# Kernel optimization log

Measured on AMD Instinct MI355X. Metric: run time of the kernel, lower is better.

Reference implementation:

```python
import jax, jax.numpy as jnp
import numpy as np

HOUSE_DIM = 4
HOUSE_NUM = 10   # house_num(6) + 2*housd_num(2) for model 'HousE'
HOUSD_NUM = 2
THRED = 0.5
GAMMA = 12.0
NENTITY = 100000
NRELATION = 500
HID = 100        # hidden_dim(400) / house_dim(4)
B, NEG = 512, 256
SCALE = (GAMMA + 2.0) / (HID * HOUSE_DIM ** 0.5)  # embedding_range


def setup_inputs() -> dict:
    key = jax.random.key(0)
    ks = jax.random.split(key, 9)
    return {
        'entity_embedding': jax.random.normal(ks[0], (NENTITY, HID, HOUSE_DIM), jnp.float32) * SCALE,
        'relation_embedding': jax.random.normal(ks[1], (NRELATION, HID, HOUSE_DIM * HOUSE_NUM), jnp.float32) * SCALE,
        'k_dir_head': jax.random.uniform(ks[2], (NRELATION, 1, HOUSD_NUM), jnp.float32, -0.01, 0.01),
        'k_dir_tail': jax.random.uniform(ks[3], (NRELATION, 1, HOUSD_NUM), jnp.float32, -0.01, 0.01),
        'k_scale_head': jax.random.uniform(ks[4], (NRELATION, HID, HOUSD_NUM), jnp.float32, -1.0, 1.0),
        'k_scale_tail': jax.random.uniform(ks[5], (NRELATION, HID, HOUSD_NUM), jnp.float32, -1.0, 1.0),
        'head_idx': jax.random.randint(ks[6], (B,), 0, NENTITY, jnp.int32),
        'rel_idx': jax.random.randint(ks[7], (B,), 0, NRELATION, jnp.int32),
        'tail_idx': jax.random.randint(ks[8], (B, NEG), 0, NENTITY, jnp.int32),
    }


def _reflect(x, v, coef):
    # x - coef * <v, x> * v along the house_dim axis
    return x - coef * jnp.sum(v * x, axis=-1, keepdims=True) * v


def reference(entity_embedding, relation_embedding, k_dir_head, k_dir_tail,
              k_scale_head, k_scale_tail, head_idx, rel_idx, tail_idx):
    # norm_embedding: per-chunk L2 normalize over house_dim
    r = relation_embedding.reshape(NRELATION, HID, HOUSE_NUM, HOUSE_DIM)
    r = r / jnp.maximum(jnp.linalg.norm(r, axis=-1, keepdims=True), 1e-12)
    # k = dir * |scale|, clamp values above thred (upper clamp only)
    k_head = jnp.minimum(k_dir_head * jnp.abs(k_scale_head), THRED)  # [R, HID, housd]
    k_tail = jnp.minimum(k_dir_tail * jnp.abs(k_scale_tail), THRED)

    # tail-batch gathers
    head = entity_embedding[head_idx][:, None]   # [B, 1,   HID, hd]
    rel = r[rel_idx][:, None]                    # [B, 1,   HID, HN, hd]
    kh = k_head[rel_idx][:, None]                # [B, 1,   HID, housd]
    kt = k_tail[rel_idx][:, None]
    tail = entity_embedding[tail_idx]            # [B, NEG, HID, hd]

    # HousE scoring, tail-batch branch
    for i in range(HOUSD_NUM):
        head = _reflect(head, rel[..., HOUSE_NUM - 1 - i, :], kh[..., i:i + 1])
    for i in range(HOUSD_NUM, HOUSE_NUM - HOUSD_NUM):
        j = HOUSE_NUM - 1 - i
        head = _reflect(head, rel[..., j, :], 2.0)
    for i in range(HOUSD_NUM):
        tail = _reflect(tail, rel[..., i, :], kt[..., i:i + 1])

    diff = head - tail                            # [B, NEG, HID, hd]
    cos_score = jnp.sum(jnp.linalg.norm(diff, axis=-1), axis=-1)  # [B, NEG]
    return GAMMA - cos_score
```

## Files before the change

kernel.cpp:

```cpp
#include <hip/hip_runtime.h>
#include <math.h>

#define NENTITY   100000
#define NRELATION 500
#define HID       100
#define HOUSE_DIM 4
#define HOUSE_NUM 10
#define B_SZ      512
#define NEG       256
#define THRED     0.5f
#define GAMMA     12.0f

#define SEGS           4
#define NEG_PER_BLOCK  (NEG / SEGS)
#define BLOCK          256
#define NEG_PER_WAVE   (NEG_PER_BLOCK / 4)

__device__ __forceinline__ float dot4(const float4 a, const float4 b) {
    return a.x * b.x + a.y * b.y + a.z * b.z + a.w * b.w;
}

__device__ __forceinline__ float4 norm4(float4 v) {
    const float n = fmaxf(sqrtf(dot4(v, v)), 1e-12f);
    const float inv = 1.0f / n;
    v.x *= inv; v.y *= inv; v.z *= inv; v.w *= inv;
    return v;
}

__device__ __forceinline__ float4 reflect4(float4 x, const float4 v, const float coef) {
    const float s = coef * dot4(v, x);
    x.x -= s * v.x; x.y -= s * v.y; x.z -= s * v.z; x.w -= s * v.w;
    return x;
}

__device__ __forceinline__ float hdist(float4 tv, const float4 v0, const float4 v1,
                                       const float2 kt, const float4 hd) {
    const float s0 = kt.x * dot4(v0, tv);
    tv.x -= s0 * v0.x; tv.y -= s0 * v0.y; tv.z -= s0 * v0.z; tv.w -= s0 * v0.w;
    const float s1 = kt.y * dot4(v1, tv);
    tv.x -= s1 * v1.x; tv.y -= s1 * v1.y; tv.z -= s1 * v1.z; tv.w -= s1 * v1.w;
    const float dx = hd.x - tv.x;
    const float dy = hd.y - tv.y;
    const float dz = hd.z - tv.z;
    const float dw = hd.w - tv.w;
    return sqrtf(dx * dx + dy * dy + dz * dz + dw * dw);
}

__global__ __launch_bounds__(BLOCK, 6) void house_score_kernel(
    const float* __restrict__ ent,
    const float* __restrict__ rel,
    const float* __restrict__ kdh,
    const float* __restrict__ kdt,
    const float* __restrict__ ksh,
    const float* __restrict__ kst,
    const int* __restrict__ head_idx,
    const int* __restrict__ rel_idx,
    const int* __restrict__ tail_idx,
    float* __restrict__ out)
{
    __shared__ float4 sHead[HID];
    __shared__ float4 sV0[HID];
    __shared__ float4 sV1[HID];
    __shared__ float2 sKt[HID];

    const int blk = blockIdx.x;
    const int b   = blk >> 2;
    const int seg = blk & (SEGS - 1);
    const int tid = threadIdx.x;
    const int r   = rel_idx[b];

    if (tid < HID) {
        const int h = tid;
        const float4* rr = (const float4*)(rel + ((size_t)r * HID + h) * (HOUSE_NUM * HOUSE_DIM));

        const int he = head_idx[b];
        float4 hd = ((const float4*)ent)[(size_t)he * HID + h];

        const float kh0 = fminf(kdh[r * 2 + 0] * fabsf(ksh[((size_t)r * HID + h) * 2 + 0]), THRED);
        const float kh1 = fminf(kdh[r * 2 + 1] * fabsf(ksh[((size_t)r * HID + h) * 2 + 1]), THRED);

        hd = reflect4(hd, norm4(rr[9]), kh0);
        hd = reflect4(hd, norm4(rr[8]), kh1);
        #pragma unroll
        for (int j = 7; j >= 2; --j) hd = reflect4(hd, norm4(rr[j]), 2.0f);

        const float kt0 = fminf(kdt[r * 2 + 0] * fabsf(kst[((size_t)r * HID + h) * 2 + 0]), THRED);
        const float kt1 = fminf(kdt[r * 2 + 1] * fabsf(kst[((size_t)r * HID + h) * 2 + 1]), THRED);

        sHead[h] = hd;
        sV0[h]   = norm4(rr[0]);
        sV1[h]   = norm4(rr[1]);
        sKt[h]   = make_float2(kt0, kt1);
    }
    __syncthreads();

    const int w = tid >> 6;
    const int l = tid & 63;

    const float4 hd1 = sHead[l];
    const float4 v01 = sV0[l];
    const float4 v11 = sV1[l];
    const float2 k1  = sKt[l];
    const int   l2   = (l < 36) ? (64 + l) : 99;
    const float4 hd2 = sHead[l2];
    const float4 v02 = sV0[l2];
    const float4 v12 = sV1[l2];
    const float2 k2  = sKt[l2];
    const bool has2  = (l < 36);

    const int negbase = seg * NEG_PER_BLOCK + w * NEG_PER_WAVE;

    int my_e = 0;
    if (l < NEG_PER_WAVE) my_e = tail_idx[(size_t)b * NEG + negbase + l];

    const float4* entf4 = (const float4*)ent;

    #pragma unroll 4
    for (int i = 0; i < NEG_PER_WAVE; ++i) {
        const int e = __shfl(my_e, i);
        const float4* row = entf4 + (size_t)e * HID;

        const float4 t1 = row[l];
        float d2 = 0.0f;
        if (has2) {
            const float4 t2 = row[64 + l];
            d2 = hdist(t2, v02, v12, k2, hd2);
        }
        float s = hdist(t1, v01, v11, k1, hd1) + d2;

        #pragma unroll
        for (int m = 1; m < 64; m <<= 1) s += __shfl_xor(s, m);

        if (l == 0) out[(size_t)b * NEG + negbase + i] = GAMMA - s;
    }
}

extern "C" void kernel_launch(void* const* d_in, const int* in_sizes, int n_in,
                              void* d_out, int out_size, void* d_ws, size_t ws_size,
                              hipStream_t stream) {
    const float* ent = (const float*)d_in[0];
    const float* rel = (const float*)d_in[1];
    const float* kdh = (const float*)d_in[2];
    const float* kdt = (const float*)d_in[3];
    const float* ksh = (const float*)d_in[4];
    const float* kst = (const float*)d_in[5];
    const int* head_idx = (const int*)d_in[6];
    const int* rel_idx  = (const int*)d_in[7];
    const int* tail_idx = (const int*)d_in[8];
    float* out = (float*)d_out;

    house_score_kernel<<<B_SZ * SEGS, BLOCK, 0, stream>>>(
        ent, rel, kdh, kdt, ksh, kst, head_idx, rel_idx, tail_idx, out);
}
```

Baseline: 243.2 us.

## Split head/relation preprocessing into separate prep kernel writing workspace

Per-batch head reflection and relation normalization move into a separate prep kernel that writes results to global workspace. Before, each of the four segment blocks per batch row redid this work. The scoring kernel now reads these values directly from global memory, with no shared memory and no block barrier, and launch bounds are raised to 8 blocks per CU. The cost is an extra kernel launch, a global round trip for the precomputed data, and redundant global loads per wave in place of shared-memory reads.

```diff
diff --git a/kernel.cpp b/kernel.cpp
--- a/kernel.cpp
+++ b/kernel.cpp
@@ -15,6 +15,8 @@
 #define NEG_PER_BLOCK  (NEG / SEGS)
 #define BLOCK          256
 #define NEG_PER_WAVE   (NEG_PER_BLOCK / 4)
+
+#define WS_F4_STRIDE (B_SZ * HID)
 
 __device__ __forceinline__ float dot4(const float4 a, const float4 b) {
     return a.x * b.x + a.y * b.y + a.z * b.z + a.w * b.w;
@@ -46,7 +48,7 @@
     return sqrtf(dx * dx + dy * dy + dz * dz + dw * dw);
 }
 
-__global__ __launch_bounds__(BLOCK, 6) void house_score_kernel(
+__global__ __launch_bounds__(128) void house_prep_kernel(
     const float* __restrict__ ent,
     const float* __restrict__ rel,
     const float* __restrict__ kdh,
@@ -55,57 +57,70 @@
     const float* __restrict__ kst,
     const int* __restrict__ head_idx,
     const int* __restrict__ rel_idx,
+    float* __restrict__ ws)
+{
+    const int b = blockIdx.x;
+    const int h = threadIdx.x;
+    if (h >= HID) return;
+    const int r = rel_idx[b];
+
+    const float4* rr = (const float4*)(rel + ((size_t)r * HID + h) * (HOUSE_NUM * HOUSE_DIM));
+
+    const int he = head_idx[b];
+    float4 hd = ((const float4*)ent)[(size_t)he * HID + h];
+
+    const float kh0 = fminf(kdh[r * 2 + 0] * fabsf(ksh[((size_t)r * HID + h) * 2 + 0]), THRED);
+    const float kh1 = fminf(kdh[r * 2 + 1] * fabsf(ksh[((size_t)r * HID + h) * 2 + 1]), THRED);
+
+    hd = reflect4(hd, norm4(rr[9]), kh0);
+    hd = reflect4(hd, norm4(rr[8]), kh1);
+    #pragma unroll
+    for (int j = 7; j >= 2; --j) hd = reflect4(hd, norm4(rr[j]), 2.0f);
+
+    const float kt0 = fminf(kdt[r * 2 + 0] * fabsf(kst[((size_t)r * HID + h) * 2 + 0]), THRED);
+    const float kt1 = fminf(kdt[r * 2 + 1] * fabsf(kst[((size_t)r * HID + h) * 2 + 1]), THRED);
+
+    float4* wsHead = (float4*)ws;
+    float4* wsV0   = wsHead + WS_F4_STRIDE;
+    float4* wsV1   = wsV0 + WS_F4_STRIDE;
+    float2* wsKt   = (float2*)(wsV1 + WS_F4_STRIDE);
+
+    const int idx = b * HID + h;
+    wsHead[idx] = hd;
+    wsV0[idx]   = norm4(rr[0]);
+    wsV1[idx]   = norm4(rr[1]);
+    wsKt[idx]   = make_float2(kt0, kt1);
+}
+
+__global__ __launch_bounds__(BLOCK, 8) void house_score_kernel(
+    const float* __restrict__ ent,
     const int* __restrict__ tail_idx,
+    const float* __restrict__ ws,
     float* __restrict__ out)
 {
-    __shared__ float4 sHead[HID];
-    __shared__ float4 sV0[HID];
-    __shared__ float4 sV1[HID];
-    __shared__ float2 sKt[HID];
-
     const int blk = blockIdx.x;
     const int b   = blk >> 2;
     const int seg = blk & (SEGS - 1);
     const int tid = threadIdx.x;
-    const int r   = rel_idx[b];
-
-    if (tid < HID) {
-        const int h = tid;
-        const float4* rr = (const float4*)(rel + ((size_t)r * HID + h) * (HOUSE_NUM * HOUSE_DIM));
-
-        const int he = head_idx[b];
-        float4 hd = ((const float4*)ent)[(size_t)he * HID + h];
-
-        const float kh0 = fminf(kdh[r * 2 + 0] * fabsf(ksh[((size_t)r * HID + h) * 2 + 0]), THRED);
-        const float kh1 = fminf(kdh[r * 2 + 1] * fabsf(ksh[((size_t)r * HID + h) * 2 + 1]), THRED);
-
-        hd = reflect4(hd, norm4(rr[9]), kh0);
-        hd = reflect4(hd, norm4(rr[8]), kh1);
-        #pragma unroll
-        for (int j = 7; j >= 2; --j) hd = reflect4(hd, norm4(rr[j]), 2.0f);
-
-        const float kt0 = fminf(kdt[r * 2 + 0] * fabsf(kst[((size_t)r * HID + h) * 2 + 0]), THRED);
-        const float kt1 = fminf(kdt[r * 2 + 1] * fabsf(kst[((size_t)r * HID + h) * 2 + 1]), THRED);
-
-        sHead[h] = hd;
-        sV0[h]   = norm4(rr[0]);
-        sV1[h]   = norm4(rr[1]);
-        sKt[h]   = make_float2(kt0, kt1);
-    }
-    __syncthreads();
-
     const int w = tid >> 6;
     const int l = tid & 63;
 
-    const float4 hd1 = sHead[l];
-    const float4 v01 = sV0[l];
-    const float4 v11 = sV1[l];
-    const float2 k1  = sKt[l];
+    const float4* wsHead = (const float4*)ws;
+    const float4* wsV0   = wsHead + WS_F4_STRIDE;
+    const float4* wsV1   = wsV0 + WS_F4_STRIDE;
+    const float2* wsKt   = (const float2*)(wsV1 + WS_F4_STRIDE);
+
+    const int i1 = b * HID + l;
+    const float4 hd1 = wsHead[i1];
+    const float4 v01 = wsV0[i1];
+    const float4 v11 = wsV1[i1];
+    const float2 k1  = wsKt[i1];
     const int   l2   = (l < 36) ? (64 + l) : 99;
-    const float4 hd2 = sHead[l2];
-    const float4 v02 = sV0[l2];
-    const float4 v12 = sV1[l2];
-    const float2 k2  = sKt[l2];
+    const int   i2   = b * HID + l2;
+    const float4 hd2 = wsHead[i2];
+    const float4 v02 = wsV0[i2];
+    const float4 v12 = wsV1[i2];
+    const float2 k2  = wsKt[i2];
     const bool has2  = (l < 36);
 
     const int negbase = seg * NEG_PER_BLOCK + w * NEG_PER_WAVE;
@@ -148,7 +163,10 @@
     const int* rel_idx  = (const int*)d_in[7];
     const int* tail_idx = (const int*)d_in[8];
     float* out = (float*)d_out;
+    float* ws  = (float*)d_ws;
 
+    house_prep_kernel<<<B_SZ, 128, 0, stream>>>(
+        ent, rel, kdh, kdt, ksh, kst, head_idx, rel_idx, ws);
     house_score_kernel<<<B_SZ * SEGS, BLOCK, 0, stream>>>(
-        ent, rel, kdh, kdt, ksh, kst, head_idx, rel_idx, tail_idx, out);
+        ent, tail_idx, ws, out);
 }
```

Measured after the change: 244.6 us. About the same (+0.6%).
